# Performance work log

Hardware: AMD Instinct MI355X
Metric: run time of the kernel (lower is better)

## Reference

```python
import jax, jax.numpy as jnp
import numpy as np

FORGET_BIAS = 1.0  # tf.nn.rnn_cell.LSTMCell default
HIDDEN = 64


def setup_inputs() -> dict:
    key = jax.random.key(0)
    k1, k2 = jax.random.split(key)
    B, T, D = 4096, 9, 512
    x = jax.random.normal(k1, (B, T, D), dtype=jnp.float32)
    # Fused LSTM kernel: [(D + H), 4H], gate order (i, j, f, o) as in TF LSTMCell
    kernel = jax.random.normal(k2, (D + HIDDEN, 4 * HIDDEN), dtype=jnp.float32) * 0.02
    bias = jnp.zeros((4 * HIDDEN,), dtype=jnp.float32)
    return {"x": x, "kernel": kernel, "bias": bias}


def _lstm_scan(x, kernel, bias):
    B, T, D = x.shape
    H = HIDDEN
    # Split kernel into input and recurrent parts for a cleaner scan body.
    Wx = kernel[:D]          # [D, 4H]
    Wh = kernel[D:]          # [H, 4H]
    # Precompute input contributions for all timesteps in one big GEMM.
    xg = jnp.einsum('btd,dg->btg', x, Wx) + bias  # [B, T, 4H]

    def step(carry, xg_t):
        c, h = carry
        gates = xg_t + h @ Wh  # [B, 4H]
        i, j, f, o = jnp.split(gates, 4, axis=-1)  # TF gate order: i, j, f, o
        c_new = jax.nn.sigmoid(f + FORGET_BIAS) * c + jax.nn.sigmoid(i) * jnp.tanh(j)
        h_new = jax.nn.sigmoid(o) * jnp.tanh(c_new)
        return (c_new, h_new), h_new

    c0 = jnp.zeros((B, H), dtype=x.dtype)
    h0 = jnp.zeros((B, H), dtype=x.dtype)
    _, hs = jax.lax.scan(step, (c0, h0), jnp.swapaxes(xg, 0, 1))  # hs: [T, B, H]
    return jnp.transpose(hs, (1, 0, 2))  # [B, T, H]


def reference(x, kernel, bias):
    return _lstm_scan(x, kernel, bias)
```

## Files before the change

### kernel.cpp

```cpp
#include <hip/hip_runtime.h>
#include <math.h>

#define T_STEPS 9
#define D_IN    512
#define HID     64
#define G4      256
#define BPB     8
#define NCH     8

typedef short  short8 __attribute__((ext_vector_type(8)));
typedef float  f32x4  __attribute__((ext_vector_type(4)));
typedef unsigned int uint;
typedef unsigned short ushort;

__device__ __forceinline__ ushort f2bf(float f) {
    uint u = __float_as_uint(f);
    u = (u + 0x7FFFu + ((u >> 16) & 1u)) >> 16;
    return (ushort)u;
}
__device__ __forceinline__ float fsig(float x) {
    return 1.0f / (1.0f + __expf(-x));
}
__device__ __forceinline__ float ftanh(float x) {
    float t = __expf(-2.0f * fabsf(x));
    float r = (1.0f - t) / (1.0f + t);
    return copysignf(r, x);
}
__device__ __forceinline__ uint cvtpk(float a, float b) {
    uint r;
    asm("v_cvt_pk_bf16_f32 %0, %1, %2" : "=v"(r) : "v"(a), "v"(b));
    return r;
}
__device__ __forceinline__ f32x4 ntload4(const float* p) {
    return __builtin_nontemporal_load((const f32x4*)p);
}

__global__ __launch_bounds__(256)
void prep_w(const float* __restrict__ kern, ushort* __restrict__ wxT,
            ushort* __restrict__ whT)
{
    const int blk = blockIdx.x;
    const int n   = threadIdx.x;
    const int krow0 = (blk < 64) ? blk * 8 : 512 + (blk - 64) * 8;
    union { ushort us[8]; short8 v; } o;
    #pragma unroll
    for (int j = 0; j < 8; ++j)
        o.us[j] = f2bf(kern[(size_t)(krow0 + j) * G4 + n]);
    if (blk < 64) *(short8*)&wxT[((size_t)blk * 256 + n) * 8] = o.v;
    else          *(short8*)&whT[((size_t)(blk - 64) * 256 + n) * 8] = o.v;
}

__global__ __launch_bounds__(256, 2)
void lstm_fused(const float* __restrict__ x, const ushort* __restrict__ wxT,
                const ushort* __restrict__ whT, const float* __restrict__ bias,
                float* __restrict__ out)
{
    __shared__ __align__(16) ushort sA[3][80 * 64];
    __shared__ __align__(16) ushort sH[1024];

    const int t = threadIdx.x;
    const int w = t >> 6, l = t & 63;
    const int lane15 = l & 15, quad = l >> 4;
    const int u = w * 16 + lane15;

    const float* xbase = x + (size_t)blockIdx.x * (72 * D_IN);
    const int sq = t & 15, ow = sq >> 1, hw = sq & 1;
    int src[5], wad[5];
    #pragma unroll
    for (int j = 0; j < 5; ++j) {
        int row = j * 16 + (t >> 4);
        int b_ = row & 7, s_ = row >> 3;
        if (s_ > 8) s_ = 8;
        src[j] = (b_ * 9 + s_) * 512 + sq * 4;
        wad[j] = row * 64 + ((ow ^ (row & 7)) << 3) + (hw << 2);
    }

    if (t < 128) {
        uint4 z = {0u, 0u, 0u, 0u};
        *(uint4*)&sH[t * 8] = z;
    }

    f32x4 svA[5], svB[5];
    #pragma unroll
    for (int j = 0; j < 5; ++j) svA[j] = ntload4(&xbase[src[j]]);
    #pragma unroll
    for (int j = 0; j < 5; ++j) svB[j] = ntload4(&xbase[src[j] + 64]);

    short8 bFb[2][2][4];
    #pragma unroll
    for (int kk = 0; kk < 2; ++kk)
        #pragma unroll
        for (int g = 0; g < 4; ++g)
            bFb[0][kk][g] = *(const short8*)
                &wxT[(size_t)((kk * 4 + quad) * 256 + g * 64 + u) * 8];

    #pragma unroll
    for (int j = 0; j < 5; ++j) {
        uint2 p;
        p.x = cvtpk(svA[j][0], svA[j][1]);
        p.y = cvtpk(svA[j][2], svA[j][3]);
        *(uint2*)&sA[0][wad[j]] = p;
    }
    #pragma unroll
    for (int j = 0; j < 5; ++j) svA[j] = ntload4(&xbase[src[j] + 128]);

    f32x4 acc[5][4];
    #pragma unroll
    for (int i = 0; i < 5; ++i)
        #pragma unroll
        for (int g = 0; g < 4; ++g)
            acc[i][g] = (f32x4){0.f, 0.f, 0.f, 0.f};

    #pragma unroll
    for (int k = 0; k < NCH; ++k) {
        if (k < NCH - 1) {
            #pragma unroll
            for (int j = 0; j < 5; ++j) {
                f32x4 v = ((k + 1) & 1) ? svB[j] : svA[j];
                uint2 p;
                p.x = cvtpk(v[0], v[1]);
                p.y = cvtpk(v[2], v[3]);
                *(uint2*)&sA[(k + 1) % 3][wad[j]] = p;
            }
        }
        if (k < NCH - 1) {
            #pragma unroll
            for (int kk = 0; kk < 2; ++kk)
                #pragma unroll
                for (int g = 0; g < 4; ++g)
                    bFb[(k + 1) & 1][kk][g] = *(const short8*)
                        &wxT[(size_t)((((k + 1) * 2 + kk) * 4 + quad) * 256
                                      + g * 64 + u) * 8];
        }
        if (k < NCH - 3) {
            #pragma unroll
            for (int j = 0; j < 5; ++j) {
                f32x4 v = ntload4(&xbase[src[j] + (k + 3) * 64]);
                if ((k + 3) & 1) svB[j] = v; else svA[j] = v;
            }
        }
        asm volatile("s_waitcnt lgkmcnt(0)" ::: "memory");
        __builtin_amdgcn_sched_barrier(0);
        __builtin_amdgcn_s_barrier();
        __builtin_amdgcn_sched_barrier(0);
        #pragma unroll
        for (int kk = 0; kk < 2; ++kk) {
            #pragma unroll
            for (int i = 0; i < 5; ++i) {
                int row = i * 16 + lane15;
                short8 aF = *(const short8*)
                    &sA[k % 3][row * 64 + (((kk * 4 + quad) ^ (row & 7)) << 3)];
                #pragma unroll
                for (int g = 0; g < 4; ++g)
                    acc[i][g] = __builtin_amdgcn_mfma_f32_16x16x32_bf16(
                        aF, bFb[k & 1][kk][g], acc[i][g], 0, 0, 0);
            }
        }
    }

    short8 whF[4][2];
    #pragma unroll
    for (int g = 0; g < 4; ++g)
        #pragma unroll
        for (int kh = 0; kh < 2; ++kh)
            whF[g][kh] = *(const short8*)
                &whT[(size_t)((kh * 4 + quad) * 256 + g * 64 + u) * 8];

    float bia[4];
    bia[0] = bias[u];
    bia[1] = bias[64 + u];
    bia[2] = bias[128 + u] + 1.0f;
    bia[3] = bias[192 + u];

    float cst[4] = {0.f, 0.f, 0.f, 0.f};
    const int b0 = blockIdx.x * BPB;

    #pragma unroll
    for (int s = 0; s < T_STEPS; ++s) {
        const int  i = s >> 1;
        const int  p = s & 1;
        const bool active = ((quad >> 1) == p);
        const int  bofs = (quad & 1) * 4;

        f32x4 g4[4];
        #pragma unroll
        for (int g = 0; g < 4; ++g)
            #pragma unroll
            for (int r = 0; r < 4; ++r)
                g4[g][r] = acc[i][g][r] + bia[g];

        short8 aF[2];
        #pragma unroll
        for (int kh = 0; kh < 2; ++kh)
            aF[kh] = *(const short8*)&sH[((kh * 4 + quad) * 16 + lane15) * 8];

        #pragma unroll
        for (int g = 0; g < 4; ++g)
            #pragma unroll
            for (int kh = 0; kh < 2; ++kh)
                g4[g] = __builtin_amdgcn_mfma_f32_16x16x32_bf16(
                    aF[kh], whF[g][kh], g4[g], 0, 0, 0);

        const int wrow = 8 * ((s + 1) & 1);
        #pragma unroll
        for (int r = 0; r < 4; ++r) {
            float cp = __shfl_xor(cst[r], 32);
            if (active) {
                float ii = fsig(g4[0][r]);
                float jj = ftanh(g4[1][r]);
                float ff = fsig(g4[2][r]);
                float oo = fsig(g4[3][r]);
                float c  = ff * cp + ii * jj;
                cst[r] = c;
                float h = oo * ftanh(c);
                int bb = bofs + r;
                __builtin_nontemporal_store(
                    h, &out[((size_t)(b0 + bb) * T_STEPS + s) * HID + u]);
                sH[((u >> 3) * 16 + wrow + bb) * 8 + (u & 7)] = f2bf(h);
            }
        }
        asm volatile("s_waitcnt lgkmcnt(0)" ::: "memory");
        __builtin_amdgcn_sched_barrier(0);
        __builtin_amdgcn_s_barrier();
        __builtin_amdgcn_sched_barrier(0);
    }
}

extern "C" void kernel_launch(void* const* d_in, const int* in_sizes, int n_in,
                              void* d_out, int out_size, void* d_ws, size_t ws_size,
                              hipStream_t stream)
{
    const float* x    = (const float*)d_in[0];
    const float* kern = (const float*)d_in[1];
    const float* bias = (const float*)d_in[2];
    float* out = (float*)d_out;

    const int B = in_sizes[0] / (T_STEPS * D_IN);

    ushort* wxT = (ushort*)d_ws;
    ushort* whT = (ushort*)((char*)d_ws + 262144);

    prep_w<<<72, 256, 0, stream>>>(kern, wxT, whT);
    lstm_fused<<<B / BPB, 256, 0, stream>>>(x, wxT, whT, bias, out);
}
```

Measured before the change: 131.5 us.

## Double batch per block and split gates across wave pairs with 512 threads

Each block now handles 16 batch rows with 512 threads. Wave pairs split the four gates: even waves compute i and j and odd waves compute f and o. The even waves pass sig(i)*tanh(j) through a new shared buffer, and the odd waves finish the cell update. This removes the idle half-wave pattern of the old recurrence and the lane shuffle for c, and it gives more MFMA work per block. The cost is an extra barrier per timestep, more shared memory and fewer blocks.

```diff
diff --git a/kernel.cpp b/kernel.cpp
--- a/kernel.cpp
+++ b/kernel.cpp
@@ -5,7 +5,9 @@
 #define D_IN    512
 #define HID     64
 #define G4      256
-#define BPB     8
+#define BPB     16
+#define TROWS   160
+#define NFRAG   9
 #define NCH     8
 
 typedef short  short8 __attribute__((ext_vector_type(8)));
@@ -50,26 +52,28 @@
     else          *(short8*)&whT[((size_t)(blk - 64) * 256 + n) * 8] = o.v;
 }
 
-__global__ __launch_bounds__(256, 2)
+__global__ __launch_bounds__(512, 2)
 void lstm_fused(const float* __restrict__ x, const ushort* __restrict__ wxT,
                 const ushort* __restrict__ whT, const float* __restrict__ bias,
                 float* __restrict__ out)
 {
-    __shared__ __align__(16) ushort sA[3][80 * 64];
+    __shared__ __align__(16) ushort sA[3][TROWS * 64];
     __shared__ __align__(16) ushort sH[1024];
+    __shared__ __align__(16) float  aX[16 * 64];
 
     const int t = threadIdx.x;
     const int w = t >> 6, l = t & 63;
     const int lane15 = l & 15, quad = l >> 4;
-    const int u = w * 16 + lane15;
-
-    const float* xbase = x + (size_t)blockIdx.x * (72 * D_IN);
+    const int un = (w >> 1) * 16 + lane15;
+    const int nb = (w & 1) * 128;
+
+    const float* xbase = x + (size_t)blockIdx.x * (BPB * T_STEPS * D_IN);
     const int sq = t & 15, ow = sq >> 1, hw = sq & 1;
     int src[5], wad[5];
     #pragma unroll
     for (int j = 0; j < 5; ++j) {
-        int row = j * 16 + (t >> 4);
-        int b_ = row & 7, s_ = row >> 3;
+        int row = j * 32 + (t >> 4);
+        int b_ = row & 15, s_ = row >> 4;
         if (s_ > 8) s_ = 8;
         src[j] = (b_ * 9 + s_) * 512 + sq * 4;
         wad[j] = row * 64 + ((ow ^ (row & 7)) << 3) + (hw << 2);
@@ -86,13 +90,13 @@
     #pragma unroll
     for (int j = 0; j < 5; ++j) svB[j] = ntload4(&xbase[src[j] + 64]);
 
-    short8 bFb[2][2][4];
+    short8 bFb[2][2][2];
     #pragma unroll
     for (int kk = 0; kk < 2; ++kk)
         #pragma unroll
-        for (int g = 0; g < 4; ++g)
+        for (int g = 0; g < 2; ++g)
             bFb[0][kk][g] = *(const short8*)
-                &wxT[(size_t)((kk * 4 + quad) * 256 + g * 64 + u) * 8];
+                &wxT[(size_t)((kk * 4 + quad) * 256 + nb + g * 64 + un) * 8];
 
     #pragma unroll
     for (int j = 0; j < 5; ++j) {
@@ -104,11 +108,11 @@
     #pragma unroll
     for (int j = 0; j < 5; ++j) svA[j] = ntload4(&xbase[src[j] + 128]);
 
-    f32x4 acc[5][4];
-    #pragma unroll
-    for (int i = 0; i < 5; ++i)
-        #pragma unroll
-        for (int g = 0; g < 4; ++g)
+    f32x4 acc[NFRAG][2];
+    #pragma unroll
+    for (int i = 0; i < NFRAG; ++i)
+        #pragma unroll
+        for (int g = 0; g < 2; ++g)
             acc[i][g] = (f32x4){0.f, 0.f, 0.f, 0.f};
 
     #pragma unroll
@@ -127,10 +131,10 @@
             #pragma unroll
             for (int kk = 0; kk < 2; ++kk)
                 #pragma unroll
-                for (int g = 0; g < 4; ++g)
+                for (int g = 0; g < 2; ++g)
                     bFb[(k + 1) & 1][kk][g] = *(const short8*)
                         &wxT[(size_t)((((k + 1) * 2 + kk) * 4 + quad) * 256
-                                      + g * 64 + u) * 8];
+                                      + nb + g * 64 + un) * 8];
         }
         if (k < NCH - 3) {
             #pragma unroll
@@ -146,48 +150,41 @@
         #pragma unroll
         for (int kk = 0; kk < 2; ++kk) {
             #pragma unroll
-            for (int i = 0; i < 5; ++i) {
+            for (int i = 0; i < NFRAG; ++i) {
                 int row = i * 16 + lane15;
                 short8 aF = *(const short8*)
                     &sA[k % 3][row * 64 + (((kk * 4 + quad) ^ (row & 7)) << 3)];
-                #pragma unroll
-                for (int g = 0; g < 4; ++g)
-                    acc[i][g] = __builtin_amdgcn_mfma_f32_16x16x32_bf16(
-                        aF, bFb[k & 1][kk][g], acc[i][g], 0, 0, 0);
-            }
-        }
-    }
-
-    short8 whF[4][2];
-    #pragma unroll
-    for (int g = 0; g < 4; ++g)
+                acc[i][0] = __builtin_amdgcn_mfma_f32_16x16x32_bf16(
+                    aF, bFb[k & 1][kk][0], acc[i][0], 0, 0, 0);
+                acc[i][1] = __builtin_amdgcn_mfma_f32_16x16x32_bf16(
+                    aF, bFb[k & 1][kk][1], acc[i][1], 0, 0, 0);
+            }
+        }
+    }
+
+    short8 whF[2][2];
+    #pragma unroll
+    for (int g = 0; g < 2; ++g)
         #pragma unroll
         for (int kh = 0; kh < 2; ++kh)
             whF[g][kh] = *(const short8*)
-                &whT[(size_t)((kh * 4 + quad) * 256 + g * 64 + u) * 8];
-
-    float bia[4];
-    bia[0] = bias[u];
-    bia[1] = bias[64 + u];
-    bia[2] = bias[128 + u] + 1.0f;
-    bia[3] = bias[192 + u];
+                &whT[(size_t)((kh * 4 + quad) * 256 + nb + g * 64 + un) * 8];
+
+    const bool oddw = (w & 1) != 0;
+    float bia0 = bias[nb + un] + (oddw ? 1.0f : 0.0f);
+    float bia1 = bias[nb + 64 + un];
 
     float cst[4] = {0.f, 0.f, 0.f, 0.f};
     const int b0 = blockIdx.x * BPB;
 
     #pragma unroll
     for (int s = 0; s < T_STEPS; ++s) {
-        const int  i = s >> 1;
-        const int  p = s & 1;
-        const bool active = ((quad >> 1) == p);
-        const int  bofs = (quad & 1) * 4;
-
-        f32x4 g4[4];
-        #pragma unroll
-        for (int g = 0; g < 4; ++g)
-            #pragma unroll
-            for (int r = 0; r < 4; ++r)
-                g4[g][r] = acc[i][g][r] + bia[g];
+        f32x4 g0, g1;
+        #pragma unroll
+        for (int r = 0; r < 4; ++r) {
+            g0[r] = acc[s][0][r] + bia0;
+            g1[r] = acc[s][1][r] + bia1;
+        }
 
         short8 aF[2];
         #pragma unroll
@@ -195,28 +192,32 @@
             aF[kh] = *(const short8*)&sH[((kh * 4 + quad) * 16 + lane15) * 8];
 
         #pragma unroll
-        for (int g = 0; g < 4; ++g)
-            #pragma unroll
-            for (int kh = 0; kh < 2; ++kh)
-                g4[g] = __builtin_amdgcn_mfma_f32_16x16x32_bf16(
-                    aF[kh], whF[g][kh], g4[g], 0, 0, 0);
-
-        const int wrow = 8 * ((s + 1) & 1);
-        #pragma unroll
-        for (int r = 0; r < 4; ++r) {
-            float cp = __shfl_xor(cst[r], 32);
-            if (active) {
-                float ii = fsig(g4[0][r]);
-                float jj = ftanh(g4[1][r]);
-                float ff = fsig(g4[2][r]);
-                float oo = fsig(g4[3][r]);
-                float c  = ff * cp + ii * jj;
+        for (int kh = 0; kh < 2; ++kh) {
+            g0 = __builtin_amdgcn_mfma_f32_16x16x32_bf16(aF[kh], whF[0][kh], g0, 0, 0, 0);
+            g1 = __builtin_amdgcn_mfma_f32_16x16x32_bf16(aF[kh], whF[1][kh], g1, 0, 0, 0);
+        }
+
+        if (!oddw) {
+            #pragma unroll
+            for (int r = 0; r < 4; ++r)
+                aX[(quad * 4 + r) * 64 + un] = fsig(g0[r]) * ftanh(g1[r]);
+        }
+        asm volatile("s_waitcnt lgkmcnt(0)" ::: "memory");
+        __builtin_amdgcn_sched_barrier(0);
+        __builtin_amdgcn_s_barrier();
+        __builtin_amdgcn_sched_barrier(0);
+
+        if (oddw) {
+            #pragma unroll
+            for (int r = 0; r < 4; ++r) {
+                float a = aX[(quad * 4 + r) * 64 + un];
+                float c = fsig(g0[r]) * cst[r] + a;
                 cst[r] = c;
-                float h = oo * ftanh(c);
-                int bb = bofs + r;
+                float h = fsig(g1[r]) * ftanh(c);
+                int bb = quad * 4 + r;
                 __builtin_nontemporal_store(
-                    h, &out[((size_t)(b0 + bb) * T_STEPS + s) * HID + u]);
-                sH[((u >> 3) * 16 + wrow + bb) * 8 + (u & 7)] = f2bf(h);
+                    h, &out[((size_t)(b0 + bb) * T_STEPS + s) * HID + un]);
+                sH[((un >> 3) * 16 + bb) * 8 + (un & 7)] = f2bf(h);
             }
         }
         asm volatile("s_waitcnt lgkmcnt(0)" ::: "memory");
@@ -241,5 +242,5 @@
     ushort* whT = (ushort*)((char*)d_ws + 262144);
 
     prep_w<<<72, 256, 0, stream>>>(kern, wxT, whT);
-    lstm_fused<<<B / BPB, 256, 0, stream>>>(x, wxT, whT, bias, out);
-}
+    lstm_fused<<<B / BPB, 512, 0, stream>>>(x, wxT, whT, bias, out);
+}
```

Result: faster. 128.5 us (-2.3%).
